# Kernel optimization log

Hardware: AMD Instinct MI355X
Metric: run time of the kernel (lower is better)

The kernel has to match this reference:

```python
import jax, jax.numpy as jnp
import numpy as np

T, H, I, E, K = 8192, 1024, 2048, 8, 2


def setup_inputs() -> dict:
    key = jax.random.key(0)
    ks = jax.random.split(key, 6)
    s_h = 1.0 / np.sqrt(H)
    s_i = 1.0 / np.sqrt(I)
    return {
        "x": jax.random.normal(ks[0], (T, H), dtype=jnp.float32),
        "Wr": jax.random.normal(ks[1], (H, E), dtype=jnp.float32) * s_h,
        "br": jnp.zeros((E,), dtype=jnp.float32),
        "Wg": jax.random.normal(ks[2], (E, H, I), dtype=jnp.float32) * s_h,
        "Wu": jax.random.normal(ks[3], (E, H, I), dtype=jnp.float32) * s_h,
        "Wd": jax.random.normal(ks[4], (E, I, H), dtype=jnp.float32) * s_i,
    }


def reference(x, Wr, br, Wg, Wu, Wd):
    # Router: dense GEMM + top-k + sigmoid gate renormalization
    logits = x @ Wr + br                            # [T, E]
    topk_vals, topk_idx = jax.lax.top_k(logits, K)  # [T, K]
    g = jax.nn.sigmoid(topk_vals)
    g = g / (jnp.sum(g, axis=-1, keepdims=True) + 1e-10)
    # Scatter gates to dense [T, E] combine weights (zero for unselected experts)
    gates = jnp.zeros((x.shape[0], Wr.shape[1]), dtype=x.dtype)
    gates = gates.at[jnp.arange(x.shape[0])[:, None], topk_idx].add(g)
    # SwiGLU expert MLP, computed densely over experts and combined by gates
    h_gate = jnp.einsum("th,ehi->tei", x, Wg)       # [T, E, I]
    h_up = jnp.einsum("th,ehi->tei", x, Wu)
    h = jax.nn.silu(h_gate) * h_up
    h = h * gates[:, :, None]                       # fuse gate combine before down-proj
    out = jnp.einsum("tei,eih->th", h, Wd)          # [T, H]
    return out
```

## Files before the change

### kernel.cpp

```cpp
#include <hip/hip_runtime.h>
#include <hip/hip_bf16.h>
#include <stdint.h>

#define TT 8192
#define HH 1024
#define II 2048
#define EE 8
#define TOPK 2

typedef __bf16 bf16x8 __attribute__((ext_vector_type(8)));
typedef float f32x4 __attribute__((ext_vector_type(4)));
typedef unsigned short us8 __attribute__((ext_vector_type(8)));

__device__ __forceinline__ unsigned short f2bf(float f) {
  union { float f; unsigned int u; } c; c.f = f;
  unsigned int u = c.u;
  u += 0x7FFFu + ((u >> 16) & 1u);
  return (unsigned short)(u >> 16);
}

__device__ __forceinline__ void gload_lds16(const void* g, void* l) {
  __builtin_amdgcn_global_load_lds((const __attribute__((address_space(1))) void*)g,
                                   (__attribute__((address_space(3))) void*)l, 16, 0, 0);
}

__global__ __launch_bounds__(256) void k_transpose_all(
    const float* __restrict__ Wg, const float* __restrict__ Wu,
    const float* __restrict__ Wd,
    unsigned short* __restrict__ WguT, unsigned short* __restrict__ WdT) {
  __shared__ float tile[64][65];
  const int job = blockIdx.y;
  const int e = blockIdx.z;
  const int x = blockIdx.x;
  const float* src; int C, r0, c0;
  if (job < 2) {
    src = (job ? Wu : Wg) + (size_t)e * HH * II;
    C = II; c0 = (x & 31) * 64; r0 = (x >> 5) * 64;
  } else {
    src = Wd + (size_t)e * II * HH;
    C = HH; c0 = (x & 15) * 64; r0 = (x >> 4) * 64;
  }
  const int tid = threadIdx.x;
  const int tx = tid & 15, ty = tid >> 4;
#pragma unroll
  for (int i = 0; i < 4; ++i) {
    int rr = i * 16 + ty;
    float4 v = *reinterpret_cast<const float4*>(&src[(size_t)(r0 + rr) * C + c0 + tx * 4]);
    tile[rr][tx * 4 + 0] = v.x; tile[rr][tx * 4 + 1] = v.y;
    tile[rr][tx * 4 + 2] = v.z; tile[rr][tx * 4 + 3] = v.w;
  }
  __syncthreads();
#pragma unroll
  for (int i = 0; i < 2; ++i) {
    int idx = i * 256 + tid;
    int cc = idx >> 3, ch = idx & 7;
    us8 o;
#pragma unroll
    for (int j = 0; j < 8; ++j) o[j] = f2bf(tile[ch * 8 + j][cc]);
    if (job < 2) {
      int srow = c0 * 2 + ((cc >> 4) << 5) + job * 16 + (cc & 15);
      *reinterpret_cast<us8*>(&WguT[((size_t)e * 2 * II + srow) * HH + r0 + ch * 8]) = o;
    } else {
      *reinterpret_cast<us8*>(&WdT[((size_t)e * HH + c0 + cc) * II + r0 + ch * 8]) = o;
    }
  }
}

__global__ __launch_bounds__(256) void k_router(const float* __restrict__ x,
                                                const float* __restrict__ Wr,
                                                const float* __restrict__ br,
                                                unsigned short* __restrict__ xb,
                                                int* __restrict__ tlist,
                                                float* __restrict__ glist,
                                                int* __restrict__ counts) {
  __shared__ float wrt[8][1024];
  __shared__ int lcount[8];
  __shared__ int lbase[8];
  __shared__ short ent_e[128];
  __shared__ short ent_slot[128];
  __shared__ float ent_g[128];
  int tid = threadIdx.x;
  for (int i = tid; i < 8192; i += 256) {
    wrt[i & 7][i >> 3] = Wr[i];
  }
  if (tid < 8) lcount[tid] = 0;
  __syncthreads();
  int w = tid >> 6, l = tid & 63;
  int t0 = blockIdx.x * 64;
  for (int it = 0; it < 16; ++it) {
    int t = t0 + w * 16 + it;
    const float4* xr = reinterpret_cast<const float4*>(x + (size_t)t * HH);
    float acc[8] = {0.f, 0.f, 0.f, 0.f, 0.f, 0.f, 0.f, 0.f};
#pragma unroll
    for (int j = 0; j < 4; ++j) {
      float4 xv = xr[j * 64 + l];
      int hbase = (j * 64 + l) * 4;
      ushort4 o;
      o.x = f2bf(xv.x); o.y = f2bf(xv.y); o.z = f2bf(xv.z); o.w = f2bf(xv.w);
      *reinterpret_cast<ushort4*>(xb + (size_t)t * HH + hbase) = o;
#pragma unroll
      for (int e = 0; e < 8; ++e) {
        float4 wv = *reinterpret_cast<const float4*>(&wrt[e][hbase]);
        acc[e] += xv.x * wv.x + xv.y * wv.y + xv.z * wv.z + xv.w * wv.w;
      }
    }
#pragma unroll
    for (int e = 0; e < 8; ++e)
#pragma unroll
      for (int off = 32; off > 0; off >>= 1) acc[e] += __shfl_xor(acc[e], off, 64);
    if (l == 0) {
      float lg[8];
#pragma unroll
      for (int e = 0; e < 8; ++e) lg[e] = acc[e] + br[e];
      int i0 = 0;
#pragma unroll
      for (int e = 1; e < 8; ++e) if (lg[e] > lg[i0]) i0 = e;
      int i1 = (i0 == 0) ? 1 : 0;
#pragma unroll
      for (int e = 0; e < 8; ++e) if (e != i0 && lg[e] > lg[i1]) i1 = e;
      float g0 = 1.f / (1.f + expf(-lg[i0]));
      float g1 = 1.f / (1.f + expf(-lg[i1]));
      float inv = 1.f / (g0 + g1 + 1e-10f);
      int idx = (w * 16 + it) * 2;
      int s0 = atomicAdd(&lcount[i0], 1);
      ent_e[idx] = (short)i0; ent_slot[idx] = (short)s0; ent_g[idx] = g0 * inv;
      int s1 = atomicAdd(&lcount[i1], 1);
      ent_e[idx + 1] = (short)i1; ent_slot[idx + 1] = (short)s1; ent_g[idx + 1] = g1 * inv;
    }
  }
  __syncthreads();
  if (tid < 8) lbase[tid] = atomicAdd(&counts[tid], lcount[tid]);
  __syncthreads();
  if (tid < 128) {
    int e = ent_e[tid];
    int slot = lbase[e] + ent_slot[tid];
    int t = t0 + (tid >> 1);
    tlist[e * TT + slot] = t;
    glist[e * TT + slot] = ent_g[tid];
  }
}

__global__ void k_offsets(const int* __restrict__ counts, int* __restrict__ offs) {
  if (threadIdx.x == 0) {
    int s = 0;
    for (int e = 0; e < EE; ++e) { offs[e] = s; s += counts[e]; }
  }
}

__global__ __launch_bounds__(256, 4) void k_gemm1(
    const unsigned short* __restrict__ xb,
    const unsigned short* __restrict__ WguT,
    const int* __restrict__ tlist, const float* __restrict__ glist,
    const int* __restrict__ counts, const int* __restrict__ offs,
    unsigned short* __restrict__ hbuf) {
  __shared__ unsigned short lsA[128 * 64];
  __shared__ unsigned short lsB[128 * 64];
  __shared__ int s_tok[128];
  __shared__ float s_gate[128];

  const int e = blockIdx.z;
  const int n_e = counts[e];
  const int row0 = blockIdx.y * 128;
  if (row0 >= n_e) return;
  const int n0 = blockIdx.x * 128;
  const int tid = threadIdx.x;

  if (tid < 128) {
    int r = row0 + tid;
    int tok = 0; float gt = 0.f;
    if (r < n_e) { tok = tlist[e * TT + r]; gt = glist[e * TT + r]; }
    s_tok[tid] = tok; s_gate[tid] = gt;
  }
  __syncthreads();

  const int scol = (tid & 7) ^ ((tid >> 3) & 7);
  const unsigned short* srcA[4];
  const unsigned short* srcB[4];
#pragma unroll
  for (int i = 0; i < 4; ++i) {
    int row = i * 32 + (tid >> 3);
    srcA[i] = xb + (size_t)s_tok[row] * HH + scol * 8;
    srcB[i] = WguT + ((size_t)e * 2 * II + n0 + row) * HH + scol * 8;
  }

  f32x4 zero = {0.f, 0.f, 0.f, 0.f};
  f32x4 acc[4][4];
#pragma unroll
  for (int m = 0; m < 4; ++m)
#pragma unroll
    for (int n = 0; n < 4; ++n) acc[m][n] = zero;

  const int l = tid & 63;
  const int w = tid >> 6;
  const int wr = (w >> 1) * 64;
  const int wc = (w & 1) * 64;
  const int lrow = l & 15;
  const int lk = l >> 4;
  const int swz = (l & 7) << 4;
  const int aoff0 = (wr + lrow) * 128 + lk * 16;
  const int boff0 = (wc + lrow) * 128 + lk * 16;
  const char* lcA = (const char*)lsA;
  const char* lcB = (const char*)lsB;

  for (int kt = 0; kt < HH / 64; ++kt) {
#pragma unroll
    for (int i = 0; i < 4; ++i) {
      gload_lds16(srcA[i] + kt * 64, (char*)lsA + i * 4096 + tid * 16);
      gload_lds16(srcB[i] + kt * 64, (char*)lsB + i * 4096 + tid * 16);
    }
    __syncthreads();
#pragma unroll
    for (int kk = 0; kk < 2; ++kk) {
      bf16x8 af[4], bf[4];
#pragma unroll
      for (int m = 0; m < 4; ++m)
        af[m] = *(const bf16x8*)(lcA + ((aoff0 + m * 2048 + kk * 64) ^ swz));
#pragma unroll
      for (int n = 0; n < 4; ++n)
        bf[n] = *(const bf16x8*)(lcB + ((boff0 + n * 2048 + kk * 64) ^ swz));
#pragma unroll
      for (int m = 0; m < 4; ++m)
#pragma unroll
        for (int n = 0; n < 4; ++n)
          acc[m][n] = __builtin_amdgcn_mfma_f32_16x16x32_bf16(af[m], bf[n], acc[m][n], 0, 0, 0);
    }
    __syncthreads();
  }

  const int obase = offs[e];
#pragma unroll
  for (int m = 0; m < 4; ++m)
#pragma unroll
    for (int n = 0; n < 4; n += 2)
#pragma unroll
      for (int r = 0; r < 4; ++r) {
        int rl = wr + m * 16 + lk * 4 + r;
        if (row0 + rl < n_e) {
          float gv = acc[m][n][r];
          float uv = acc[m][n + 1][r];
          float val = gv / (1.f + __expf(-gv)) * uv * s_gate[rl];
          int L = (n0 >> 1) + (wc >> 1) + (n >> 1) * 16 + lrow;
          hbuf[(size_t)(obase + row0 + rl) * II + L] = f2bf(val);
        }
      }
}

__global__ __launch_bounds__(256, 4) void k_gemm2(
    const unsigned short* __restrict__ hbuf,
    const unsigned short* __restrict__ WdT,
    const int* __restrict__ tlist,
    const int* __restrict__ counts, const int* __restrict__ offs,
    float* __restrict__ out) {
  __shared__ unsigned short lsA[128 * 64];
  __shared__ unsigned short lsB[128 * 64];
  __shared__ int s_tok[128];

  const int e = blockIdx.z;
  const int n_e = counts[e];
  const int row0 = blockIdx.y * 128;
  if (row0 >= n_e) return;
  const int n0 = blockIdx.x * 128;
  const int tid = threadIdx.x;
  const int obase = offs[e];

  if (tid < 128) {
    int r = row0 + tid;
    s_tok[tid] = (r < n_e) ? tlist[e * TT + r] : 0;
  }
  __syncthreads();

  const int scol = (tid & 7) ^ ((tid >> 3) & 7);
  const unsigned short* srcA[4];
  const unsigned short* srcB[4];
#pragma unroll
  for (int i = 0; i < 4; ++i) {
    int row = i * 32 + (tid >> 3);
    int ar = obase + row0 + row;
    if (ar > TT * TOPK - 1) ar = TT * TOPK - 1;
    srcA[i] = hbuf + (size_t)ar * II + scol * 8;
    srcB[i] = WdT + ((size_t)e * HH + n0 + row) * II + scol * 8;
  }

  f32x4 zero = {0.f, 0.f, 0.f, 0.f};
  f32x4 acc[4][4];
#pragma unroll
  for (int m = 0; m < 4; ++m)
#pragma unroll
    for (int n = 0; n < 4; ++n) acc[m][n] = zero;

  const int l = tid & 63;
  const int w = tid >> 6;
  const int wr = (w >> 1) * 64;
  const int wc = (w & 1) * 64;
  const int lrow = l & 15;
  const int lk = l >> 4;
  const int swz = (l & 7) << 4;
  const int aoff0 = (wr + lrow) * 128 + lk * 16;
  const int boff0 = (wc + lrow) * 128 + lk * 16;
  const char* lcA = (const char*)lsA;
  const char* lcB = (const char*)lsB;

  for (int kt = 0; kt < II / 64; ++kt) {
#pragma unroll
    for (int i = 0; i < 4; ++i) {
      gload_lds16(srcA[i] + kt * 64, (char*)lsA + i * 4096 + tid * 16);
      gload_lds16(srcB[i] + kt * 64, (char*)lsB + i * 4096 + tid * 16);
    }
    __syncthreads();
#pragma unroll
    for (int kk = 0; kk < 2; ++kk) {
      bf16x8 af[4], bf[4];
#pragma unroll
      for (int m = 0; m < 4; ++m)
        af[m] = *(const bf16x8*)(lcA + ((aoff0 + m * 2048 + kk * 64) ^ swz));
#pragma unroll
      for (int n = 0; n < 4; ++n)
        bf[n] = *(const bf16x8*)(lcB + ((boff0 + n * 2048 + kk * 64) ^ swz));
#pragma unroll
      for (int m = 0; m < 4; ++m)
#pragma unroll
        for (int n = 0; n < 4; ++n)
          acc[m][n] = __builtin_amdgcn_mfma_f32_16x16x32_bf16(af[m], bf[n], acc[m][n], 0, 0, 0);
    }
    __syncthreads();
  }

#pragma unroll
  for (int m = 0; m < 4; ++m)
#pragma unroll
    for (int n = 0; n < 4; ++n)
#pragma unroll
      for (int r = 0; r < 4; ++r) {
        int rl = wr + m * 16 + lk * 4 + r;
        if (row0 + rl < n_e) {
          int t = s_tok[rl];
          unsafeAtomicAdd(&out[(size_t)t * HH + n0 + wc + n * 16 + lrow], acc[m][n][r]);
        }
      }
}

extern "C" void kernel_launch(void* const* d_in, const int* in_sizes, int n_in,
                              void* d_out, int out_size, void* d_ws, size_t ws_size,
                              hipStream_t stream) {
  const float* x  = (const float*)d_in[0];
  const float* Wr = (const float*)d_in[1];
  const float* br = (const float*)d_in[2];
  const float* Wg = (const float*)d_in[3];
  const float* Wu = (const float*)d_in[4];
  const float* Wd = (const float*)d_in[5];
  float* out = (float*)d_out;

  char* ws = (char*)d_ws;
  size_t off = 0;
  auto alloc = [&](size_t bytes) {
    char* p = ws + off;
    off += (bytes + 255) & ~(size_t)255;
    return p;
  };
  unsigned short* xb   = (unsigned short*)alloc((size_t)TT * HH * 2);
  unsigned short* WguT = (unsigned short*)alloc((size_t)EE * 2 * II * HH * 2);
  unsigned short* WdT  = (unsigned short*)alloc((size_t)EE * HH * II * 2);
  unsigned short* hbuf = (unsigned short*)alloc((size_t)TT * TOPK * II * 2);
  int*   tlist  = (int*)alloc((size_t)EE * TT * 4);
  float* glist  = (float*)alloc((size_t)EE * TT * 4);
  int*   counts = (int*)alloc(128);
  int*   offs   = (int*)alloc(128);

  hipMemsetAsync(counts, 0, 128, stream);
  hipMemsetAsync(d_out, 0, (size_t)TT * HH * 4, stream);

  dim3 tall(512, 3, EE);
  k_transpose_all<<<tall, 256, 0, stream>>>(Wg, Wu, Wd, WguT, WdT);

  k_router<<<TT / 64, 256, 0, stream>>>(x, Wr, br, xb, tlist, glist, counts);
  k_offsets<<<1, 64, 0, stream>>>(counts, offs);

  dim3 g1(2 * II / 128, TT / 128, EE);
  k_gemm1<<<g1, 256, 0, stream>>>(xb, WguT, tlist, glist, counts, offs, hbuf);
  dim3 g2(HH / 128, TT / 128, EE);
  k_gemm2<<<g2, 256, 0, stream>>>(hbuf, WdT, tlist, counts, offs, out);

  (void)in_sizes; (void)n_in; (void)out_size; (void)ws_size;
}
```

Baseline: 381.2 us.

## Merge router and weight transpose into one prep kernel, drop offsets kernel

```diff
diff --git a/kernel.cpp b/kernel.cpp
--- a/kernel.cpp
+++ b/kernel.cpp
@@ -24,30 +24,113 @@
                                    (__attribute__((address_space(3))) void*)l, 16, 0, 0);
 }
 
-__global__ __launch_bounds__(256) void k_transpose_all(
+struct RouterSm {
+  float wrt[8][1024];
+  int lcount[8];
+  int lbase[8];
+  short ent_e[128];
+  short ent_slot[128];
+  float ent_g[128];
+};
+struct TransSm {
+  float tile[64][65];
+};
+
+__global__ __launch_bounds__(256) void k_prep(
+    const float* __restrict__ x, const float* __restrict__ Wr,
+    const float* __restrict__ br,
     const float* __restrict__ Wg, const float* __restrict__ Wu,
     const float* __restrict__ Wd,
-    unsigned short* __restrict__ WguT, unsigned short* __restrict__ WdT) {
-  __shared__ float tile[64][65];
-  const int job = blockIdx.y;
-  const int e = blockIdx.z;
-  const int x = blockIdx.x;
+    unsigned short* __restrict__ xb,
+    unsigned short* __restrict__ WguT, unsigned short* __restrict__ WdT,
+    int* __restrict__ tlist, float* __restrict__ glist,
+    int* __restrict__ counts) {
+  __shared__ __align__(16) char smem[sizeof(RouterSm)];
+  const int bid = blockIdx.x;
+  const int tid = threadIdx.x;
+
+  if (bid < 128) {
+    RouterSm& R = *reinterpret_cast<RouterSm*>(smem);
+    for (int i = tid; i < 8192; i += 256) R.wrt[i & 7][i >> 3] = Wr[i];
+    if (tid < 8) R.lcount[tid] = 0;
+    __syncthreads();
+    int w = tid >> 6, l = tid & 63;
+    int t0 = bid * 64;
+    for (int it = 0; it < 16; ++it) {
+      int t = t0 + w * 16 + it;
+      const float4* xr = reinterpret_cast<const float4*>(x + (size_t)t * HH);
+      float acc[8] = {0.f, 0.f, 0.f, 0.f, 0.f, 0.f, 0.f, 0.f};
+#pragma unroll
+      for (int j = 0; j < 4; ++j) {
+        float4 xv = xr[j * 64 + l];
+        int hbase = (j * 64 + l) * 4;
+        ushort4 o;
+        o.x = f2bf(xv.x); o.y = f2bf(xv.y); o.z = f2bf(xv.z); o.w = f2bf(xv.w);
+        *reinterpret_cast<ushort4*>(xb + (size_t)t * HH + hbase) = o;
+#pragma unroll
+        for (int e = 0; e < 8; ++e) {
+          float4 wv = *reinterpret_cast<const float4*>(&R.wrt[e][hbase]);
+          acc[e] += xv.x * wv.x + xv.y * wv.y + xv.z * wv.z + xv.w * wv.w;
+        }
+      }
+#pragma unroll
+      for (int e = 0; e < 8; ++e)
+#pragma unroll
+        for (int off = 32; off > 0; off >>= 1) acc[e] += __shfl_xor(acc[e], off, 64);
+      if (l == 0) {
+        float lg[8];
+#pragma unroll
+        for (int e = 0; e < 8; ++e) lg[e] = acc[e] + br[e];
+        int i0 = 0;
+#pragma unroll
+        for (int e = 1; e < 8; ++e) if (lg[e] > lg[i0]) i0 = e;
+        int i1 = (i0 == 0) ? 1 : 0;
+#pragma unroll
+        for (int e = 0; e < 8; ++e) if (e != i0 && lg[e] > lg[i1]) i1 = e;
+        float g0 = 1.f / (1.f + expf(-lg[i0]));
+        float g1 = 1.f / (1.f + expf(-lg[i1]));
+        float inv = 1.f / (g0 + g1 + 1e-10f);
+        int idx = (w * 16 + it) * 2;
+        int s0 = atomicAdd(&R.lcount[i0], 1);
+        R.ent_e[idx] = (short)i0; R.ent_slot[idx] = (short)s0; R.ent_g[idx] = g0 * inv;
+        int s1 = atomicAdd(&R.lcount[i1], 1);
+        R.ent_e[idx + 1] = (short)i1; R.ent_slot[idx + 1] = (short)s1; R.ent_g[idx + 1] = g1 * inv;
+      }
+    }
+    __syncthreads();
+    if (tid < 8) R.lbase[tid] = atomicAdd(&counts[tid], R.lcount[tid]);
+    __syncthreads();
+    if (tid < 128) {
+      int e = R.ent_e[tid];
+      int slot = R.lbase[e] + R.ent_slot[tid];
+      int t = t0 + (tid >> 1);
+      tlist[e * TT + slot] = t;
+      glist[e * TT + slot] = R.ent_g[tid];
+    }
+    return;
+  }
+
+  TransSm& T = *reinterpret_cast<TransSm*>(smem);
+  const int tb = bid - 128;
+  const int job = tb / 4096;
+  const int rem = tb - job * 4096;
+  const int e = rem >> 9;
+  const int xt = rem & 511;
   const float* src; int C, r0, c0;
   if (job < 2) {
     src = (job ? Wu : Wg) + (size_t)e * HH * II;
-    C = II; c0 = (x & 31) * 64; r0 = (x >> 5) * 64;
+    C = II; c0 = (xt & 31) * 64; r0 = (xt >> 5) * 64;
   } else {
     src = Wd + (size_t)e * II * HH;
-    C = HH; c0 = (x & 15) * 64; r0 = (x >> 4) * 64;
-  }
-  const int tid = threadIdx.x;
+    C = HH; c0 = (xt & 15) * 64; r0 = (xt >> 4) * 64;
+  }
   const int tx = tid & 15, ty = tid >> 4;
 #pragma unroll
   for (int i = 0; i < 4; ++i) {
     int rr = i * 16 + ty;
     float4 v = *reinterpret_cast<const float4*>(&src[(size_t)(r0 + rr) * C + c0 + tx * 4]);
-    tile[rr][tx * 4 + 0] = v.x; tile[rr][tx * 4 + 1] = v.y;
-    tile[rr][tx * 4 + 2] = v.z; tile[rr][tx * 4 + 3] = v.w;
+    T.tile[rr][tx * 4 + 0] = v.x; T.tile[rr][tx * 4 + 1] = v.y;
+    T.tile[rr][tx * 4 + 2] = v.z; T.tile[rr][tx * 4 + 3] = v.w;
   }
   __syncthreads();
 #pragma unroll
@@ -56,7 +139,7 @@
     int cc = idx >> 3, ch = idx & 7;
     us8 o;
 #pragma unroll
-    for (int j = 0; j < 8; ++j) o[j] = f2bf(tile[ch * 8 + j][cc]);
+    for (int j = 0; j < 8; ++j) o[j] = f2bf(T.tile[ch * 8 + j][cc]);
     if (job < 2) {
       int srow = c0 * 2 + ((cc >> 4) << 5) + job * 16 + (cc & 15);
       *reinterpret_cast<us8*>(&WguT[((size_t)e * 2 * II + srow) * HH + r0 + ch * 8]) = o;
@@ -66,92 +149,11 @@
   }
 }
 
-__global__ __launch_bounds__(256) void k_router(const float* __restrict__ x,
-                                                const float* __restrict__ Wr,
-                                                const float* __restrict__ br,
-                                                unsigned short* __restrict__ xb,
-                                                int* __restrict__ tlist,
-                                                float* __restrict__ glist,
-                                                int* __restrict__ counts) {
-  __shared__ float wrt[8][1024];
-  __shared__ int lcount[8];
-  __shared__ int lbase[8];
-  __shared__ short ent_e[128];
-  __shared__ short ent_slot[128];
-  __shared__ float ent_g[128];
-  int tid = threadIdx.x;
-  for (int i = tid; i < 8192; i += 256) {
-    wrt[i & 7][i >> 3] = Wr[i];
-  }
-  if (tid < 8) lcount[tid] = 0;
-  __syncthreads();
-  int w = tid >> 6, l = tid & 63;
-  int t0 = blockIdx.x * 64;
-  for (int it = 0; it < 16; ++it) {
-    int t = t0 + w * 16 + it;
-    const float4* xr = reinterpret_cast<const float4*>(x + (size_t)t * HH);
-    float acc[8] = {0.f, 0.f, 0.f, 0.f, 0.f, 0.f, 0.f, 0.f};
-#pragma unroll
-    for (int j = 0; j < 4; ++j) {
-      float4 xv = xr[j * 64 + l];
-      int hbase = (j * 64 + l) * 4;
-      ushort4 o;
-      o.x = f2bf(xv.x); o.y = f2bf(xv.y); o.z = f2bf(xv.z); o.w = f2bf(xv.w);
-      *reinterpret_cast<ushort4*>(xb + (size_t)t * HH + hbase) = o;
-#pragma unroll
-      for (int e = 0; e < 8; ++e) {
-        float4 wv = *reinterpret_cast<const float4*>(&wrt[e][hbase]);
-        acc[e] += xv.x * wv.x + xv.y * wv.y + xv.z * wv.z + xv.w * wv.w;
-      }
-    }
-#pragma unroll
-    for (int e = 0; e < 8; ++e)
-#pragma unroll
-      for (int off = 32; off > 0; off >>= 1) acc[e] += __shfl_xor(acc[e], off, 64);
-    if (l == 0) {
-      float lg[8];
-#pragma unroll
-      for (int e = 0; e < 8; ++e) lg[e] = acc[e] + br[e];
-      int i0 = 0;
-#pragma unroll
-      for (int e = 1; e < 8; ++e) if (lg[e] > lg[i0]) i0 = e;
-      int i1 = (i0 == 0) ? 1 : 0;
-#pragma unroll
-      for (int e = 0; e < 8; ++e) if (e != i0 && lg[e] > lg[i1]) i1 = e;
-      float g0 = 1.f / (1.f + expf(-lg[i0]));
-      float g1 = 1.f / (1.f + expf(-lg[i1]));
-      float inv = 1.f / (g0 + g1 + 1e-10f);
-      int idx = (w * 16 + it) * 2;
-      int s0 = atomicAdd(&lcount[i0], 1);
-      ent_e[idx] = (short)i0; ent_slot[idx] = (short)s0; ent_g[idx] = g0 * inv;
-      int s1 = atomicAdd(&lcount[i1], 1);
-      ent_e[idx + 1] = (short)i1; ent_slot[idx + 1] = (short)s1; ent_g[idx + 1] = g1 * inv;
-    }
-  }
-  __syncthreads();
-  if (tid < 8) lbase[tid] = atomicAdd(&counts[tid], lcount[tid]);
-  __syncthreads();
-  if (tid < 128) {
-    int e = ent_e[tid];
-    int slot = lbase[e] + ent_slot[tid];
-    int t = t0 + (tid >> 1);
-    tlist[e * TT + slot] = t;
-    glist[e * TT + slot] = ent_g[tid];
-  }
-}
-
-__global__ void k_offsets(const int* __restrict__ counts, int* __restrict__ offs) {
-  if (threadIdx.x == 0) {
-    int s = 0;
-    for (int e = 0; e < EE; ++e) { offs[e] = s; s += counts[e]; }
-  }
-}
-
 __global__ __launch_bounds__(256, 4) void k_gemm1(
     const unsigned short* __restrict__ xb,
     const unsigned short* __restrict__ WguT,
     const int* __restrict__ tlist, const float* __restrict__ glist,
-    const int* __restrict__ counts, const int* __restrict__ offs,
+    const int* __restrict__ counts,
     unsigned short* __restrict__ hbuf) {
   __shared__ unsigned short lsA[128 * 64];
   __shared__ unsigned short lsB[128 * 64];
@@ -159,10 +161,16 @@
   __shared__ float s_gate[128];
 
   const int e = blockIdx.z;
-  const int n_e = counts[e];
-  const int row0 = blockIdx.y * 128;
+  int n_e = 0, obase = 0;
+#pragma unroll
+  for (int q = 0; q < EE; ++q) {
+    int c = counts[q];
+    if (q < e) obase += c;
+    if (q == e) n_e = c;
+  }
+  const int row0 = blockIdx.x * 128;
   if (row0 >= n_e) return;
-  const int n0 = blockIdx.x * 128;
+  const int n0 = blockIdx.y * 128;
   const int tid = threadIdx.x;
 
   if (tid < 128) {
@@ -227,7 +235,6 @@
     __syncthreads();
   }
 
-  const int obase = offs[e];
 #pragma unroll
   for (int m = 0; m < 4; ++m)
 #pragma unroll
@@ -249,19 +256,24 @@
     const unsigned short* __restrict__ hbuf,
     const unsigned short* __restrict__ WdT,
     const int* __restrict__ tlist,
-    const int* __restrict__ counts, const int* __restrict__ offs,
+    const int* __restrict__ counts,
     float* __restrict__ out) {
   __shared__ unsigned short lsA[128 * 64];
   __shared__ unsigned short lsB[128 * 64];
   __shared__ int s_tok[128];
 
   const int e = blockIdx.z;
-  const int n_e = counts[e];
-  const int row0 = blockIdx.y * 128;
+  int n_e = 0, obase = 0;
+#pragma unroll
+  for (int q = 0; q < EE; ++q) {
+    int c = counts[q];
+    if (q < e) obase += c;
+    if (q == e) n_e = c;
+  }
+  const int row0 = blockIdx.x * 128;
   if (row0 >= n_e) return;
-  const int n0 = blockIdx.x * 128;
+  const int n0 = blockIdx.y * 128;
   const int tid = threadIdx.x;
-  const int obase = offs[e];
 
   if (tid < 128) {
     int r = row0 + tid;
@@ -364,21 +376,17 @@
   int*   tlist  = (int*)alloc((size_t)EE * TT * 4);
   float* glist  = (float*)alloc((size_t)EE * TT * 4);
   int*   counts = (int*)alloc(128);
-  int*   offs   = (int*)alloc(128);
 
   hipMemsetAsync(counts, 0, 128, stream);
   hipMemsetAsync(d_out, 0, (size_t)TT * HH * 4, stream);
 
-  dim3 tall(512, 3, EE);
-  k_transpose_all<<<tall, 256, 0, stream>>>(Wg, Wu, Wd, WguT, WdT);
-
-  k_router<<<TT / 64, 256, 0, stream>>>(x, Wr, br, xb, tlist, glist, counts);
-  k_offsets<<<1, 64, 0, stream>>>(counts, offs);
-
-  dim3 g1(2 * II / 128, TT / 128, EE);
-  k_gemm1<<<g1, 256, 0, stream>>>(xb, WguT, tlist, glist, counts, offs, hbuf);
-  dim3 g2(HH / 128, TT / 128, EE);
-  k_gemm2<<<g2, 256, 0, stream>>>(hbuf, WdT, tlist, counts, offs, out);
+  k_prep<<<128 + 3 * EE * 512, 256, 0, stream>>>(x, Wr, br, Wg, Wu, Wd,
+                                                 xb, WguT, WdT, tlist, glist, counts);
+
+  dim3 g1(TT / 128, 2 * II / 128, EE);
+  k_gemm1<<<g1, 256, 0, stream>>>(xb, WguT, tlist, glist, counts, hbuf);
+  dim3 g2(TT / 128, HH / 128, EE);
+  k_gemm2<<<g2, 256, 0, stream>>>(hbuf, WdT, tlist, counts, out);
 
   (void)in_sizes; (void)n_in; (void)out_size; (void)ws_size;
 }
```

Result: slower. 444.0 us (+16.5%).
